# Performance work log

Hardware: AMD Instinct MI355X
Metric: run time of the kernel (lower is better)

Reference implementation:

```python
import jax, jax.numpy as jnp
import numpy as np

N_USERS = 100000
EMBED = 128
N_EDGES = 1_600_000  # avg degree 16


def setup_inputs() -> dict:
    key = jax.random.key(0)
    k1, k2, k3, k4, k5 = jax.random.split(key, 5)
    s_rows = jnp.sort(jax.random.randint(k1, (N_EDGES,), 0, N_USERS))
    s_cols = jax.random.randint(k2, (N_EDGES,), 0, N_USERS)
    # row-normalization D^-1 A, matching the scipy preprocessing in __init__
    deg = jax.ops.segment_sum(jnp.ones((N_EDGES,), jnp.float32), s_rows, num_segments=N_USERS)
    deg = jnp.where(deg == 0, 1.0, deg)
    s_values = 1.0 / deg[s_rows]
    user_embeds = jax.random.normal(k3, (N_USERS, EMBED), jnp.float32) * 0.1
    bound = float(np.sqrt(6.0 / (EMBED + EMBED)))  # xavier_uniform
    W0 = jax.random.uniform(k4, (EMBED, EMBED), jnp.float32, -bound, bound)
    W1 = jax.random.uniform(k5, (EMBED, EMBED), jnp.float32, -bound, bound)
    return {"user_embeds": user_embeds, "s_rows": s_rows, "s_cols": s_cols,
            "s_values": s_values, "W0": W0, "W1": W1}


def reference(user_embeds, s_rows, s_cols, s_values, W0, W1):
    # SocialGCN.forward: per layer x_new = x + dropout(S @ (x @ W_l));
    # dropout is identity in eval mode. Returns all layer outputs (stacked).
    n_users = user_embeds.shape[0]
    outs = [user_embeds]
    x = user_embeds
    for W in (W0, W1):
        xt = x @ W  # [n_users, d] dense GEMM
        # SpMM: out[r] = sum_{e: rows[e]==r} vals[e] * xt[cols[e]]
        msg = s_values[:, None] * xt[s_cols]  # [n_edges, d] irregular gather
        agg = jax.ops.segment_sum(msg, s_rows, num_segments=n_users)
        x = x + agg  # residual add
        outs.append(x)
    return jnp.stack(outs)  # [n_layers+1, n_users, d]
```

## Files before the change

kernel.cpp:

```cpp
#include <hip/hip_runtime.h>

#define N_USERS  100000
#define EMBED    128

typedef __attribute__((ext_vector_type(8))) short bf16x8;
typedef __attribute__((ext_vector_type(4))) float f32x4;

__global__ __launch_bounds__(256) void rowptr_kernel(const int* __restrict__ rows,
                                                     int* __restrict__ row_ptr,
                                                     int n_rows, int n_edges) {
  int r = blockIdx.x * blockDim.x + threadIdx.x;
  if (r > n_rows) return;
  int lo = 0, hi = n_edges;
  while (lo < hi) {
    int mid = (lo + hi) >> 1;
    if (rows[mid] < r) lo = mid + 1; else hi = mid;
  }
  row_ptr[r] = lo;
}

__global__ __launch_bounds__(256) void wconv_kernel(const float* __restrict__ W0,
                                                    const float* __restrict__ W1,
                                                    uint* __restrict__ Wt0,
                                                    uint* __restrict__ Wt1) {
  const float* W  = blockIdx.x ? W1 : W0;
  uint*        Wt = blockIdx.x ? Wt1 : Wt0;
  for (int idx = threadIdx.x; idx < 128 * 64; idx += 256) {
    int n = idx >> 6;
    int kp = idx & 63;
    float a = W[(2 * kp) * 128 + n];
    float b = W[(2 * kp + 1) * 128 + n];
    uint o;
    asm("v_cvt_pk_bf16_f32 %0, %1, %2" : "=v"(o) : "v"(a), "v"(b));
    Wt[n * 64 + kp] = o;
  }
}

__global__ __launch_bounds__(256) void gemm_kernel(const float* __restrict__ X,
                                                   const ushort* __restrict__ Wt,
                                                   unsigned char* __restrict__ Y8,
                                                   float* __restrict__ scale_arr,
                                                   float* __restrict__ Xcopy) {
  const int tid  = threadIdx.x;
  const int wave = tid >> 6;
  const int lane = tid & 63;
  const int l15  = lane & 15;
  const int lg   = lane >> 4;
  const int m    = blockIdx.x * 64 + wave * 16 + l15;
  const int mc   = m < N_USERS ? m : N_USERS - 1;
  const bool act = m < N_USERS;
  const float* xrow = X + (size_t)mc * EMBED;

  f32x4 acc[8];
  #pragma unroll
  for (int t = 0; t < 8; ++t) acc[t] = (f32x4){0.f, 0.f, 0.f, 0.f};

  #pragma unroll
  for (int s = 0; s < 4; ++s) {
    const int k0 = s * 32 + lg * 8;
    float4 xa = *(const float4*)(xrow + k0);
    float4 xb = *(const float4*)(xrow + k0 + 4);
    if (Xcopy && act) {
      *(float4*)(Xcopy + (size_t)m * EMBED + k0)     = xa;
      *(float4*)(Xcopy + (size_t)m * EMBED + k0 + 4) = xb;
    }
    union { bf16x8 v; uint u[4]; } bfr;
    asm("v_cvt_pk_bf16_f32 %0, %1, %2" : "=v"(bfr.u[0]) : "v"(xa.x), "v"(xa.y));
    asm("v_cvt_pk_bf16_f32 %0, %1, %2" : "=v"(bfr.u[1]) : "v"(xa.z), "v"(xa.w));
    asm("v_cvt_pk_bf16_f32 %0, %1, %2" : "=v"(bfr.u[2]) : "v"(xb.x), "v"(xb.y));
    asm("v_cvt_pk_bf16_f32 %0, %1, %2" : "=v"(bfr.u[3]) : "v"(xb.z), "v"(xb.w));
    #pragma unroll
    for (int nt = 0; nt < 8; ++nt) {
      union { bf16x8 v; uint4 u; } afr;
      afr.u = *(const uint4*)(Wt + (size_t)(nt * 16 + l15) * 128 + k0);
      acc[nt] = __builtin_amdgcn_mfma_f32_16x16x32_bf16(afr.v, bfr.v, acc[nt], 0, 0, 0);
    }
  }

  if (act) {
    float amax = 0.f;
    #pragma unroll
    for (int nt = 0; nt < 8; ++nt)
      #pragma unroll
      for (int i = 0; i < 4; ++i) amax = fmaxf(amax, fabsf(acc[nt][i]));
    amax = fmaxf(amax, __shfl_xor(amax, 16));
    amax = fmaxf(amax, __shfl_xor(amax, 32));
    const float inv = amax > 0.f ? 127.0f / amax : 0.f;
    if (lg == 0) scale_arr[m] = amax * (1.0f / 127.0f);

    unsigned char* yrow = Y8 + (size_t)m * EMBED;
    #pragma unroll
    for (int nt = 0; nt < 8; ++nt) {
      uint q = 0;
      #pragma unroll
      for (int i = 0; i < 4; ++i) {
        int qi = __float2int_rn(acc[nt][i] * inv) + 128;
        q |= (uint)qi << (8 * i);
      }
      *(uint*)(yrow + nt * 16 + lg * 4) = q;
    }
  }
}

__device__ __forceinline__ void fma16(float* acc, uint4 g, float vs) {
  float f;
  #define CVT_ACC(word, b, slot)                                        \
    asm("v_cvt_f32_ubyte" #b " %0, %1" : "=v"(f) : "v"(word));          \
    acc[slot] = fmaf(vs, f, acc[slot]);
  CVT_ACC(g.x, 0, 0)  CVT_ACC(g.x, 1, 1)  CVT_ACC(g.x, 2, 2)  CVT_ACC(g.x, 3, 3)
  CVT_ACC(g.y, 0, 4)  CVT_ACC(g.y, 1, 5)  CVT_ACC(g.y, 2, 6)  CVT_ACC(g.y, 3, 7)
  CVT_ACC(g.z, 0, 8)  CVT_ACC(g.z, 1, 9)  CVT_ACC(g.z, 2, 10) CVT_ACC(g.z, 3, 11)
  CVT_ACC(g.w, 0, 12) CVT_ACC(g.w, 1, 13) CVT_ACC(g.w, 2, 14) CVT_ACC(g.w, 3, 15)
  #undef CVT_ACC
}

__global__ __launch_bounds__(256) void spmm_kernel(const unsigned char* __restrict__ XT8,
                                                   const float* __restrict__ scale_arr,
                                                   const float* __restrict__ X,
                                                   const int* __restrict__ row_ptr,
                                                   const int* __restrict__ cols,
                                                   const float* __restrict__ vals,
                                                   float* __restrict__ OUT) {
  const int tid = threadIdx.x;
  const int l   = tid & 7;
  const int rg  = tid >> 3;
  const int row = blockIdx.x * 32 + rg;
  if (row >= N_USERS) return;
  const int start = row_ptr[row];
  const int end   = row_ptr[row + 1];
  const uint4* XT4 = (const uint4*)XT8;

  float acc[16];
  #pragma unroll
  for (int j = 0; j < 16; ++j) acc[j] = 0.f;
  float vsum = 0.f;

  int e = start;
  int e_pre = (start + 3) & ~3;
  if (e_pre > end) e_pre = end;
  for (; e < e_pre; ++e) {
    int c = cols[e];
    float vs = vals[e] * scale_arr[c];
    vsum += vs;
    fma16(acc, XT4[(size_t)c * 8 + l], vs);
  }
  for (; e + 4 <= end; e += 4) {
    int4   ca = *(const int4*)(cols + e);
    float4 va = *(const float4*)(vals + e);
    float s0 = scale_arr[ca.x], s1 = scale_arr[ca.y];
    float s2 = scale_arr[ca.z], s3 = scale_arr[ca.w];
    uint4 g0 = XT4[(size_t)ca.x * 8 + l];
    uint4 g1 = XT4[(size_t)ca.y * 8 + l];
    uint4 g2 = XT4[(size_t)ca.z * 8 + l];
    uint4 g3 = XT4[(size_t)ca.w * 8 + l];
    float vs0 = va.x * s0, vs1 = va.y * s1, vs2 = va.z * s2, vs3 = va.w * s3;
    vsum += vs0 + vs1 + vs2 + vs3;
    fma16(acc, g0, vs0);
    fma16(acc, g1, vs1);
    fma16(acc, g2, vs2);
    fma16(acc, g3, vs3);
  }
  for (; e < end; ++e) {
    int c = cols[e];
    float vs = vals[e] * scale_arr[c];
    vsum += vs;
    fma16(acc, XT4[(size_t)c * 8 + l], vs);
  }

  const float corr = vsum * 128.0f;
  const float* xr = X + (size_t)row * EMBED + l * 16;
  float*       orow = OUT + (size_t)row * EMBED + l * 16;
  #pragma unroll
  for (int k = 0; k < 4; ++k) {
    float4 r = *(const float4*)(xr + k * 4);
    float4 o = {acc[k * 4 + 0] - corr + r.x,
                acc[k * 4 + 1] - corr + r.y,
                acc[k * 4 + 2] - corr + r.z,
                acc[k * 4 + 3] - corr + r.w};
    *(float4*)(orow + k * 4) = o;
  }
}

extern "C" void kernel_launch(void* const* d_in, const int* in_sizes, int n_in,
                              void* d_out, int out_size, void* d_ws, size_t ws_size,
                              hipStream_t stream) {
  const float* user_embeds = (const float*)d_in[0];
  const int*   s_rows      = (const int*)d_in[1];
  const int*   s_cols      = (const int*)d_in[2];
  const float* s_values    = (const float*)d_in[3];
  const float* W0          = (const float*)d_in[4];
  const float* W1          = (const float*)d_in[5];
  float* out = (float*)d_out;

  const int n_edges = in_sizes[1];
  const size_t layer = (size_t)N_USERS * EMBED;

  char* ws = (char*)d_ws;
  unsigned char* xt8 = (unsigned char*)ws;  ws += layer;
  float*  scale_arr  = (float*)ws;          ws += N_USERS * sizeof(float);
  ushort* Wt0        = (ushort*)ws;         ws += 128 * 128 * sizeof(ushort);
  ushort* Wt1        = (ushort*)ws;         ws += 128 * 128 * sizeof(ushort);
  int*    row_ptr    = (int*)ws;

  rowptr_kernel<<<(N_USERS + 1 + 255) / 256, 256, 0, stream>>>(
      s_rows, row_ptr, N_USERS, n_edges);
  wconv_kernel<<<2, 256, 0, stream>>>(W0, W1, (uint*)Wt0, (uint*)Wt1);

  const ushort* Wtl[2] = {Wt0, Wt1};
  for (int l = 0; l < 2; ++l) {
    const float* Xl = (l == 0) ? user_embeds : (out + l * layer);
    gemm_kernel<<<(N_USERS + 63) / 64, 256, 0, stream>>>(
        Xl, Wtl[l], xt8, scale_arr, l == 0 ? out : nullptr);
    spmm_kernel<<<(N_USERS + 31) / 32, 256, 0, stream>>>(
        xt8, scale_arr, Xl, row_ptr, s_cols, s_values, out + (l + 1) * layer);
  }
}
```

Baseline: 201.1 us.

## Fuse layer-1 SpMM with layer-2 GEMM and quantization in one kernel

Adds a kernel that performs the first layer's sparse aggregation and residual add, writes the output, then immediately converts the row to bf16 and runs the second layer's MFMA GEMM with int8 quantization. This removes a separate GEMM launch and the re-read of the layer-1 output from memory. Double-buffered quantized/scale workspaces are used. The fused kernel maps one row per lane within 16-lane groups, which changes the gather access pattern and may hurt coalescing and balance across rows.

```diff
diff --git a/kernel.cpp b/kernel.cpp
--- a/kernel.cpp
+++ b/kernel.cpp
@@ -95,6 +95,147 @@
       #pragma unroll
       for (int i = 0; i < 4; ++i) {
         int qi = __float2int_rn(acc[nt][i] * inv) + 128;
+        q |= (uint)qi << (8 * i);
+      }
+      *(uint*)(yrow + nt * 16 + lg * 4) = q;
+    }
+  }
+}
+
+__device__ __forceinline__ void fma8b(float* a, uint2 g, float vs) {
+  float f;
+  #define CVT_ACC(word, b, slot)                                        \
+    asm("v_cvt_f32_ubyte" #b " %0, %1" : "=v"(f) : "v"(word));          \
+    a[slot] = fmaf(vs, f, a[slot]);
+  CVT_ACC(g.x, 0, 0) CVT_ACC(g.x, 1, 1) CVT_ACC(g.x, 2, 2) CVT_ACC(g.x, 3, 3)
+  CVT_ACC(g.y, 0, 4) CVT_ACC(g.y, 1, 5) CVT_ACC(g.y, 2, 6) CVT_ACC(g.y, 3, 7)
+  #undef CVT_ACC
+}
+
+__global__ __launch_bounds__(256) void spmm_fused_kernel(
+    const unsigned char* __restrict__ XT8, const float* __restrict__ scale_in,
+    const float* __restrict__ X, const int* __restrict__ row_ptr,
+    const int* __restrict__ cols, const float* __restrict__ vals,
+    const ushort* __restrict__ Wt, float* __restrict__ OUT,
+    unsigned char* __restrict__ Y8, float* __restrict__ scale_out) {
+  const int tid  = threadIdx.x;
+  const int wave = tid >> 6;
+  const int lane = tid & 63;
+  const int l15  = lane & 15;
+  const int lg   = lane >> 4;
+  const int row  = blockIdx.x * 64 + wave * 16 + l15;
+  const int rowc = row < N_USERS ? row : N_USERS - 1;
+  const bool act = row < N_USERS;
+  const int start = row_ptr[rowc];
+  const int end   = row_ptr[rowc + 1];
+
+  float acc[4][8];
+  #pragma unroll
+  for (int s = 0; s < 4; ++s)
+    #pragma unroll
+    for (int j = 0; j < 8; ++j) acc[s][j] = 0.f;
+  float vsum = 0.f;
+
+  const uint2* base2 = (const uint2*)XT8;
+  int e = start;
+  int e_pre = (start + 3) & ~3;
+  if (e_pre > end) e_pre = end;
+  for (; e < e_pre; ++e) {
+    int c = cols[e];
+    float vs = vals[e] * scale_in[c];
+    vsum += vs;
+    const uint2* src = base2 + (size_t)c * 16 + lg;
+    uint2 g0 = src[0], g1 = src[4], g2 = src[8], g3 = src[12];
+    fma8b(acc[0], g0, vs); fma8b(acc[1], g1, vs);
+    fma8b(acc[2], g2, vs); fma8b(acc[3], g3, vs);
+  }
+  for (; e + 4 <= end; e += 4) {
+    int4   ca = *(const int4*)(cols + e);
+    float4 va = *(const float4*)(vals + e);
+    float vs0 = va.x * scale_in[ca.x], vs1 = va.y * scale_in[ca.y];
+    float vs2 = va.z * scale_in[ca.z], vs3 = va.w * scale_in[ca.w];
+    vsum += vs0 + vs1 + vs2 + vs3;
+    const uint2* s0 = base2 + (size_t)ca.x * 16 + lg;
+    const uint2* s1 = base2 + (size_t)ca.y * 16 + lg;
+    const uint2* s2 = base2 + (size_t)ca.z * 16 + lg;
+    const uint2* s3 = base2 + (size_t)ca.w * 16 + lg;
+    uint2 a0 = s0[0], a1 = s0[4], a2 = s0[8],  a3 = s0[12];
+    uint2 b0 = s1[0], b1 = s1[4], b2 = s1[8],  b3 = s1[12];
+    uint2 c0 = s2[0], c1 = s2[4], c2 = s2[8],  c3 = s2[12];
+    uint2 d0 = s3[0], d1 = s3[4], d2 = s3[8],  d3 = s3[12];
+    fma8b(acc[0], a0, vs0); fma8b(acc[1], a1, vs0);
+    fma8b(acc[2], a2, vs0); fma8b(acc[3], a3, vs0);
+    fma8b(acc[0], b0, vs1); fma8b(acc[1], b1, vs1);
+    fma8b(acc[2], b2, vs1); fma8b(acc[3], b3, vs1);
+    fma8b(acc[0], c0, vs2); fma8b(acc[1], c1, vs2);
+    fma8b(acc[2], c2, vs2); fma8b(acc[3], c3, vs2);
+    fma8b(acc[0], d0, vs3); fma8b(acc[1], d1, vs3);
+    fma8b(acc[2], d2, vs3); fma8b(acc[3], d3, vs3);
+  }
+  for (; e < end; ++e) {
+    int c = cols[e];
+    float vs = vals[e] * scale_in[c];
+    vsum += vs;
+    const uint2* src = base2 + (size_t)c * 16 + lg;
+    uint2 g0 = src[0], g1 = src[4], g2 = src[8], g3 = src[12];
+    fma8b(acc[0], g0, vs); fma8b(acc[1], g1, vs);
+    fma8b(acc[2], g2, vs); fma8b(acc[3], g3, vs);
+  }
+
+  const float corr = vsum * 128.0f;
+  union { bf16x8 v; uint4 u; } bfr[4];
+  #pragma unroll
+  for (int s = 0; s < 4; ++s) {
+    const float* xr = X + (size_t)rowc * EMBED + s * 32 + lg * 8;
+    float4 ra = *(const float4*)xr;
+    float4 rb = *(const float4*)(xr + 4);
+    float o0 = acc[s][0] - corr + ra.x, o1 = acc[s][1] - corr + ra.y;
+    float o2 = acc[s][2] - corr + ra.z, o3 = acc[s][3] - corr + ra.w;
+    float o4 = acc[s][4] - corr + rb.x, o5 = acc[s][5] - corr + rb.y;
+    float o6 = acc[s][6] - corr + rb.z, o7 = acc[s][7] - corr + rb.w;
+    if (act) {
+      float* orow = OUT + (size_t)row * EMBED + s * 32 + lg * 8;
+      *(float4*)orow       = (float4){o0, o1, o2, o3};
+      *(float4*)(orow + 4) = (float4){o4, o5, o6, o7};
+    }
+    asm("v_cvt_pk_bf16_f32 %0, %1, %2" : "=v"(bfr[s].u.x) : "v"(o0), "v"(o1));
+    asm("v_cvt_pk_bf16_f32 %0, %1, %2" : "=v"(bfr[s].u.y) : "v"(o2), "v"(o3));
+    asm("v_cvt_pk_bf16_f32 %0, %1, %2" : "=v"(bfr[s].u.z) : "v"(o4), "v"(o5));
+    asm("v_cvt_pk_bf16_f32 %0, %1, %2" : "=v"(bfr[s].u.w) : "v"(o6), "v"(o7));
+  }
+
+  f32x4 accg[8];
+  #pragma unroll
+  for (int t = 0; t < 8; ++t) accg[t] = (f32x4){0.f, 0.f, 0.f, 0.f};
+  #pragma unroll
+  for (int s = 0; s < 4; ++s) {
+    const int k0 = s * 32 + lg * 8;
+    #pragma unroll
+    for (int nt = 0; nt < 8; ++nt) {
+      union { bf16x8 v; uint4 u; } afr;
+      afr.u = *(const uint4*)(Wt + (size_t)(nt * 16 + l15) * 128 + k0);
+      accg[nt] = __builtin_amdgcn_mfma_f32_16x16x32_bf16(afr.v, bfr[s].v, accg[nt], 0, 0, 0);
+    }
+  }
+
+  if (act) {
+    float amax = 0.f;
+    #pragma unroll
+    for (int nt = 0; nt < 8; ++nt)
+      #pragma unroll
+      for (int i = 0; i < 4; ++i) amax = fmaxf(amax, fabsf(accg[nt][i]));
+    amax = fmaxf(amax, __shfl_xor(amax, 16));
+    amax = fmaxf(amax, __shfl_xor(amax, 32));
+    const float inv = amax > 0.f ? 127.0f / amax : 0.f;
+    if (lg == 0) scale_out[row] = amax * (1.0f / 127.0f);
+
+    unsigned char* yrow = Y8 + (size_t)row * EMBED;
+    #pragma unroll
+    for (int nt = 0; nt < 8; ++nt) {
+      uint q = 0;
+      #pragma unroll
+      for (int i = 0; i < 4; ++i) {
+        int qi = __float2int_rn(accg[nt][i] * inv) + 128;
         q |= (uint)qi << (8 * i);
       }
       *(uint*)(yrow + nt * 16 + lg * 4) = q;
@@ -147,13 +288,12 @@
   for (; e + 4 <= end; e += 4) {
     int4   ca = *(const int4*)(cols + e);
     float4 va = *(const float4*)(vals + e);
-    float s0 = scale_arr[ca.x], s1 = scale_arr[ca.y];
-    float s2 = scale_arr[ca.z], s3 = scale_arr[ca.w];
+    float vs0 = va.x * scale_arr[ca.x], vs1 = va.y * scale_arr[ca.y];
+    float vs2 = va.z * scale_arr[ca.z], vs3 = va.w * scale_arr[ca.w];
     uint4 g0 = XT4[(size_t)ca.x * 8 + l];
     uint4 g1 = XT4[(size_t)ca.y * 8 + l];
     uint4 g2 = XT4[(size_t)ca.z * 8 + l];
     uint4 g3 = XT4[(size_t)ca.w * 8 + l];
-    float vs0 = va.x * s0, vs1 = va.y * s1, vs2 = va.z * s2, vs3 = va.w * s3;
     vsum += vs0 + vs1 + vs2 + vs3;
     fma16(acc, g0, vs0);
     fma16(acc, g1, vs1);
@@ -196,22 +336,23 @@
   const size_t layer = (size_t)N_USERS * EMBED;
 
   char* ws = (char*)d_ws;
-  unsigned char* xt8 = (unsigned char*)ws;  ws += layer;
-  float*  scale_arr  = (float*)ws;          ws += N_USERS * sizeof(float);
-  ushort* Wt0        = (ushort*)ws;         ws += 128 * 128 * sizeof(ushort);
-  ushort* Wt1        = (ushort*)ws;         ws += 128 * 128 * sizeof(ushort);
-  int*    row_ptr    = (int*)ws;
+  unsigned char* xt8a = (unsigned char*)ws;  ws += layer;
+  unsigned char* xt8b = (unsigned char*)ws;  ws += layer;
+  float*  scale_a = (float*)ws;              ws += N_USERS * sizeof(float);
+  float*  scale_b = (float*)ws;              ws += N_USERS * sizeof(float);
+  ushort* Wt0     = (ushort*)ws;             ws += 128 * 128 * sizeof(ushort);
+  ushort* Wt1     = (ushort*)ws;             ws += 128 * 128 * sizeof(ushort);
+  int*    row_ptr = (int*)ws;
 
   rowptr_kernel<<<(N_USERS + 1 + 255) / 256, 256, 0, stream>>>(
       s_rows, row_ptr, N_USERS, n_edges);
   wconv_kernel<<<2, 256, 0, stream>>>(W0, W1, (uint*)Wt0, (uint*)Wt1);
 
-  const ushort* Wtl[2] = {Wt0, Wt1};
-  for (int l = 0; l < 2; ++l) {
-    const float* Xl = (l == 0) ? user_embeds : (out + l * layer);
-    gemm_kernel<<<(N_USERS + 63) / 64, 256, 0, stream>>>(
-        Xl, Wtl[l], xt8, scale_arr, l == 0 ? out : nullptr);
-    spmm_kernel<<<(N_USERS + 31) / 32, 256, 0, stream>>>(
-        xt8, scale_arr, Xl, row_ptr, s_cols, s_values, out + (l + 1) * layer);
-  }
-}
+  gemm_kernel<<<(N_USERS + 63) / 64, 256, 0, stream>>>(
+      user_embeds, Wt0, xt8a, scale_a, out);
+  spmm_fused_kernel<<<(N_USERS + 63) / 64, 256, 0, stream>>>(
+      xt8a, scale_a, user_embeds, row_ptr, s_cols, s_values, Wt1,
+      out + layer, xt8b, scale_b);
+  spmm_kernel<<<(N_USERS + 31) / 32, 256, 0, stream>>>(
+      xt8b, scale_b, out + layer, row_ptr, s_cols, s_values, out + 2 * layer);
+}
```

Result: slower. 226.5 us (+12.6%).
